# Kernel tuning notes

Hardware: AMD Instinct MI355X
Metric: run time of the kernel (lower is better)

## Reference

```python
import jax, jax.numpy as jnp
import numpy as np

# Architecture constants (from LocalGLMnet defaults)
LOOK_BACK, N_AGES, PAD = 10, 100, 2
KH, KW = 5, 5
H_OUT, W_OUT = LOOK_BACK + 2 * PAD - KH + 1, N_AGES + 2 * PAD - KW + 1  # 10, 100
ETA, ALPHA = 0.01, 0.0  # Ridge penalty
BATCH = 16384


def setup_inputs() -> dict:
    key = jax.random.key(0)
    k1, k2 = jax.random.split(key)
    x = jax.random.normal(k1, (BATCH, LOOK_BACK, N_AGES), dtype=jnp.float32)
    # unshared locally-connected weight (H_out, W_out, kH, kW); channels are 1 and squeezed
    weight = jax.random.normal(k2, (H_OUT, W_OUT, KH, KW), dtype=jnp.float32) * 0.01
    return {"x": x, "weight": weight}


def _locally_connected(x_pad, weight):
    # x_pad: (B, H_pad, W_pad); weight: (H_out, W_out, kH, kW)
    # out[b,i,j] = sum_{di,dj} x_pad[b,i+di,j+dj] * weight[i,j,di,dj]
    # Loop only over the fixed 5x5 kernel taps (25 fused shifted multiplies),
    # avoiding materialization of a (B, H_out, W_out, 25) patch tensor.
    out = jnp.zeros((x_pad.shape[0], H_OUT, W_OUT), dtype=x_pad.dtype)
    for di in range(KH):
        for dj in range(KW):
            out = out + x_pad[:, di:di + H_OUT, dj:dj + W_OUT] * weight[:, :, di, dj]
    return jax.nn.sigmoid(out)


def reference(x, weight):
    # x: (B, look_back, n_ages)
    x_pad = jnp.pad(x, ((0, 0), (PAD, PAD), (PAD, PAD)))
    interim = _locally_connected(x_pad, weight)        # (B, 10, 100) attention coeffs
    decoded = x * interim
    forecast = jnp.sum(decoded, axis=1, keepdims=True)  # (B, 1, 100)
    eps = 1e-6
    pen = ETA * ALPHA * jnp.sqrt(interim * interim + eps) \
        + ETA * (1.0 - ALPHA) * (interim * interim)
    penalty = jnp.sum(pen, axis=1, keepdims=True)       # (B, 1, 100)
    return jnp.concatenate([forecast, penalty], axis=1)  # (B, 2, 100)
```

## Files before the change

### kernel.cpp

```cpp
#include <hip/hip_runtime.h>


#define L2E 1.44269504088896340736f

__device__ __forceinline__ float fast_sigmoid(float s) {
    float e = __builtin_amdgcn_exp2f(s * (-L2E));
    return __builtin_amdgcn_rcpf(1.0f + e);
}

#define G_DECL(S) \
    float s##S##0=0.f,s##S##1=0.f,s##S##2=0.f,s##S##3=0.f,s##S##4=0.f, \
          s##S##5=0.f,s##S##6=0.f,s##S##7=0.f,s##S##8=0.f,s##S##9=0.f; \
    float f##S=0.f, p##S=0.f, cen1##S=0.f, cen2##S=0.f; \
    float xr##S##0, xr##S##1, xr##S##2, xr##S##3, xr##S##4;

#define G_LOADROW(S, R) { \
    const float* rp_ = x##S + (R) * 100; \
    xr##S##0 = v0 ? rp_[c0] : 0.f; \
    xr##S##1 = v1 ? rp_[c1] : 0.f; \
    xr##S##2 = rp_[c2]; \
    xr##S##3 = v3 ? rp_[c3] : 0.f; \
    xr##S##4 = v4 ? rp_[c4] : 0.f; }

#define G_LOADALL(R) G_LOADROW(A,R) G_LOADROW(B,R) G_LOADROW(C,R) G_LOADROW(D,R)

#define G_ACC_(S, I) \
    s##S##I = fmaf(xr##S##4, w4_, fmaf(xr##S##3, w3_, fmaf(xr##S##2, w2_, \
              fmaf(xr##S##1, w1_, fmaf(xr##S##0, w0_, s##S##I)))));
#define G_ACC(S, I) G_ACC_(S, I)

#define G_TAP(DI, I) { \
    const float* wp_ = wj + (I) * 1250 + (DI) * 5; \
    const float w0_=wp_[0], w1_=wp_[1], w2_=wp_[2], w3_=wp_[3], w4_=wp_[4]; \
    G_ACC(A, I) G_ACC(B, I) G_ACC(C, I) G_ACC(D, I) }

#define G_FIN1_(S, I, CEN) { \
    float itm_ = fast_sigmoid(s##S##I); \
    f##S = fmaf(CEN, itm_, f##S); \
    p##S = fmaf(0.01f * itm_, itm_, p##S); }
#define G_FIN1(S, I, CEN) G_FIN1_(S, I, CEN)

#define G_FINALL(I) G_FIN1(A,I,cen2A) G_FIN1(B,I,cen2B) G_FIN1(C,I,cen2C) G_FIN1(D,I,cen2D)

#define G_SHIFT(S) cen2##S = cen1##S; cen1##S = xr##S##2;
#define G_SHIFTALL() G_SHIFT(A) G_SHIFT(B) G_SHIFT(C) G_SHIFT(D)

__global__ __launch_bounds__(256)
void glm_fused(const float* __restrict__ x, const float* __restrict__ w,
               float* __restrict__ out) {
    __shared__ float wl[12500];

    const int tid = threadIdx.x;
    const int jh  = blockIdx.x & 1;
    const int blk = blockIdx.x >> 1;

    {
        const float2* __restrict__ src = (const float2*)w;
        float2* dst = (float2*)wl;
        for (int u = tid; u < 6250; u += 256) {
            int i  = u / 625;
            int r2 = u - i * 625;
            dst[i * 625 + r2] = src[i * 1250 + jh * 625 + r2];
        }
    }
    __syncthreads();

    const int tl = blk * 256 + tid;
    const int jl = tl % 50;
    const int bg = tl / 50;
    const int j  = jh * 50 + jl;

    const float* __restrict__ xA = x + bg * 4000;
    const float* __restrict__ xB = xA + 1000;
    const float* __restrict__ xC = xA + 2000;
    const float* __restrict__ xD = xA + 3000;
    const float* __restrict__ wj = wl + jl * 25;

    const bool v0 = (j >= 2), v1 = (j >= 1), v3 = (j <= 98), v4 = (j <= 97);
    const int c0 = v0 ? j - 2 : 0;
    const int c1 = v1 ? j - 1 : 0;
    const int c2 = j;
    const int c3 = v3 ? j + 1 : 0;
    const int c4 = v4 ? j + 2 : 0;

    G_DECL(A) G_DECL(B) G_DECL(C) G_DECL(D)

    G_LOADALL(0) G_TAP(0,2) G_TAP(1,1) G_TAP(2,0)                               G_SHIFTALL()
    G_LOADALL(1) G_TAP(0,3) G_TAP(1,2) G_TAP(2,1) G_TAP(3,0)                    G_SHIFTALL()
    G_LOADALL(2) G_TAP(0,4) G_TAP(1,3) G_TAP(2,2) G_TAP(3,1) G_TAP(4,0) G_FINALL(0) G_SHIFTALL()
    G_LOADALL(3) G_TAP(0,5) G_TAP(1,4) G_TAP(2,3) G_TAP(3,2) G_TAP(4,1) G_FINALL(1) G_SHIFTALL()
    G_LOADALL(4) G_TAP(0,6) G_TAP(1,5) G_TAP(2,4) G_TAP(3,3) G_TAP(4,2) G_FINALL(2) G_SHIFTALL()
    G_LOADALL(5) G_TAP(0,7) G_TAP(1,6) G_TAP(2,5) G_TAP(3,4) G_TAP(4,3) G_FINALL(3) G_SHIFTALL()
    G_LOADALL(6) G_TAP(0,8) G_TAP(1,7) G_TAP(2,6) G_TAP(3,5) G_TAP(4,4) G_FINALL(4) G_SHIFTALL()
    G_LOADALL(7) G_TAP(0,9) G_TAP(1,8) G_TAP(2,7) G_TAP(3,6) G_TAP(4,5) G_FINALL(5) G_SHIFTALL()
    G_LOADALL(8)            G_TAP(1,9) G_TAP(2,8) G_TAP(3,7) G_TAP(4,6) G_FINALL(6) G_SHIFTALL()
    G_LOADALL(9)                       G_TAP(2,9) G_TAP(3,8) G_TAP(4,7) G_FINALL(7) G_SHIFTALL()
    G_FIN1(A,8,cen2A) G_FIN1(B,8,cen2B) G_FIN1(C,8,cen2C) G_FIN1(D,8,cen2D)
    G_FIN1(A,9,cen1A) G_FIN1(B,9,cen1B) G_FIN1(C,9,cen1C) G_FIN1(D,9,cen1D)

    float* ob = out + bg * 800 + j;
    ob[0]   = fA;  ob[100] = pA;
    ob[200] = fB;  ob[300] = pB;
    ob[400] = fC;  ob[500] = pC;
    ob[600] = fD;  ob[700] = pD;
}

extern "C" void kernel_launch(void* const* d_in, const int* in_sizes, int n_in,
                              void* d_out, int out_size, void* d_ws, size_t ws_size,
                              hipStream_t stream) {
    const float* x = (const float*)d_in[0];
    const float* w = (const float*)d_in[1];
    float* out = (float*)d_out;
    dim3 grid(1600), block(256);
    hipLaunchKernelGGL(glm_fused, grid, block, 0, stream, x, w, out);
}
```

Measured before the change: 161.3 us.

## Split columns into quarters, fold edge masks into weights, double-buffer row loads

```diff
diff --git a/kernel.cpp b/kernel.cpp
--- a/kernel.cpp
+++ b/kernel.cpp
@@ -8,101 +8,101 @@
     return __builtin_amdgcn_rcpf(1.0f + e);
 }
 
-#define G_DECL(S) \
-    float s##S##0=0.f,s##S##1=0.f,s##S##2=0.f,s##S##3=0.f,s##S##4=0.f, \
-          s##S##5=0.f,s##S##6=0.f,s##S##7=0.f,s##S##8=0.f,s##S##9=0.f; \
-    float f##S=0.f, p##S=0.f, cen1##S=0.f, cen2##S=0.f; \
-    float xr##S##0, xr##S##1, xr##S##2, xr##S##3, xr##S##4;
+#define P_LOAD_(P, R) \
+    xA0##P = aA0[(R)*100]; xA1##P = aA1[(R)*100]; xA2##P = aA2[(R)*100]; \
+    xA3##P = aA3[(R)*100]; xA4##P = aA4[(R)*100]; \
+    xB0##P = aB0[(R)*100]; xB1##P = aB1[(R)*100]; xB2##P = aB2[(R)*100]; \
+    xB3##P = aB3[(R)*100]; xB4##P = aB4[(R)*100];
+#define P_LOAD(P, R) P_LOAD_(P, R)
 
-#define G_LOADROW(S, R) { \
-    const float* rp_ = x##S + (R) * 100; \
-    xr##S##0 = v0 ? rp_[c0] : 0.f; \
-    xr##S##1 = v1 ? rp_[c1] : 0.f; \
-    xr##S##2 = rp_[c2]; \
-    xr##S##3 = v3 ? rp_[c3] : 0.f; \
-    xr##S##4 = v4 ? rp_[c4] : 0.f; }
+#define G_TAP_(P, DI, I) { \
+    const float4 w4_ = W4p[(I)*125 + (DI)]; \
+    const float  we_ = W1p[(I)*125 + (DI)]; \
+    sA##I = fmaf(xA4##P, we_, fmaf(xA3##P, w4_.w, fmaf(xA2##P, w4_.z, \
+            fmaf(xA1##P, w4_.y, fmaf(xA0##P, w4_.x, sA##I))))); \
+    sB##I = fmaf(xB4##P, we_, fmaf(xB3##P, w4_.w, fmaf(xB2##P, w4_.z, \
+            fmaf(xB1##P, w4_.y, fmaf(xB0##P, w4_.x, sB##I))))); }
+#define G_TAP(P, DI, I) G_TAP_(P, DI, I)
 
-#define G_LOADALL(R) G_LOADROW(A,R) G_LOADROW(B,R) G_LOADROW(C,R) G_LOADROW(D,R)
+#define G_FIN_(I, CA, CB) { \
+    float tA_ = fast_sigmoid(sA##I); fA = fmaf(CA, tA_, fA); pA = fmaf(0.01f*tA_, tA_, pA); \
+    float tB_ = fast_sigmoid(sB##I); fB = fmaf(CB, tB_, fB); pB = fmaf(0.01f*tB_, tB_, pB); }
+#define G_FIN(I, CA, CB) G_FIN_(I, CA, CB)
 
-#define G_ACC_(S, I) \
-    s##S##I = fmaf(xr##S##4, w4_, fmaf(xr##S##3, w3_, fmaf(xr##S##2, w2_, \
-              fmaf(xr##S##1, w1_, fmaf(xr##S##0, w0_, s##S##I)))));
-#define G_ACC(S, I) G_ACC_(S, I)
-
-#define G_TAP(DI, I) { \
-    const float* wp_ = wj + (I) * 1250 + (DI) * 5; \
-    const float w0_=wp_[0], w1_=wp_[1], w2_=wp_[2], w3_=wp_[3], w4_=wp_[4]; \
-    G_ACC(A, I) G_ACC(B, I) G_ACC(C, I) G_ACC(D, I) }
-
-#define G_FIN1_(S, I, CEN) { \
-    float itm_ = fast_sigmoid(s##S##I); \
-    f##S = fmaf(CEN, itm_, f##S); \
-    p##S = fmaf(0.01f * itm_, itm_, p##S); }
-#define G_FIN1(S, I, CEN) G_FIN1_(S, I, CEN)
-
-#define G_FINALL(I) G_FIN1(A,I,cen2A) G_FIN1(B,I,cen2B) G_FIN1(C,I,cen2C) G_FIN1(D,I,cen2D)
-
-#define G_SHIFT(S) cen2##S = cen1##S; cen1##S = xr##S##2;
-#define G_SHIFTALL() G_SHIFT(A) G_SHIFT(B) G_SHIFT(C) G_SHIFT(D)
+#define G_SH_(P) cen2A = cen1A; cen1A = xA2##P; cen2B = cen1B; cen1B = xB2##P;
+#define G_SH(P) G_SH_(P)
 
 __global__ __launch_bounds__(256)
 void glm_fused(const float* __restrict__ x, const float* __restrict__ w,
                float* __restrict__ out) {
-    __shared__ float wl[12500];
+    __shared__ float4 W4s[1250];
+    __shared__ float  W1s[1250];
 
-    const int tid = threadIdx.x;
-    const int jh  = blockIdx.x & 1;
-    const int blk = blockIdx.x >> 1;
+    const int tid   = threadIdx.x;
+    const int q     = blockIdx.x & 3;
+    const int jbase = q * 25;
 
-    {
-        const float2* __restrict__ src = (const float2*)w;
-        float2* dst = (float2*)wl;
-        for (int u = tid; u < 6250; u += 256) {
-            int i  = u / 625;
-            int r2 = u - i * 625;
-            dst[i * 625 + r2] = src[i * 1250 + jh * 625 + r2];
-        }
+    for (int e = tid; e < 1250; e += 256) {
+        int i   = e / 125;
+        int r   = e - i * 125;
+        int jls = r / 5;
+        int di  = r - jls * 5;
+        int js  = jbase + jls;
+        const float* wp = w + i * 2500 + js * 25 + di * 5;
+        float w0 = (js >= 2) ? wp[0] : 0.f;
+        float w1 = (js >= 1) ? wp[1] : 0.f;
+        float w2 = wp[2];
+        float w3 = (js <= 98) ? wp[3] : 0.f;
+        float w4 = (js <= 97) ? wp[4] : 0.f;
+        W4s[e] = make_float4(w0, w1, w2, w3);
+        W1s[e] = w4;
     }
     __syncthreads();
 
-    const int tl = blk * 256 + tid;
-    const int jl = tl % 50;
-    const int bg = tl / 50;
-    const int j  = jh * 50 + jl;
+    const int t  = (blockIdx.x >> 2) * 256 + tid;
+    const int jl = t % 25;
+    const int bg = t / 25;
+    const int j  = jbase + jl;
 
-    const float* __restrict__ xA = x + bg * 4000;
-    const float* __restrict__ xB = xA + 1000;
-    const float* __restrict__ xC = xA + 2000;
-    const float* __restrict__ xD = xA + 3000;
-    const float* __restrict__ wj = wl + jl * 25;
+    const float4* W4p = W4s + jl * 5;
+    const float*  W1p = W1s + jl * 5;
 
-    const bool v0 = (j >= 2), v1 = (j >= 1), v3 = (j <= 98), v4 = (j <= 97);
-    const int c0 = v0 ? j - 2 : 0;
-    const int c1 = v1 ? j - 1 : 0;
+    const float* xA = x + bg * 2000;
+    const float* xB = xA + 1000;
+    const int c0 = (j >= 2) ? j - 2 : 0;
+    const int c1 = (j >= 1) ? j - 1 : 0;
     const int c2 = j;
-    const int c3 = v3 ? j + 1 : 0;
-    const int c4 = v4 ? j + 2 : 0;
+    const int c3 = (j <= 98) ? j + 1 : 99;
+    const int c4 = (j <= 97) ? j + 2 : 99;
+    const float* aA0 = xA + c0; const float* aA1 = xA + c1; const float* aA2 = xA + c2;
+    const float* aA3 = xA + c3; const float* aA4 = xA + c4;
+    const float* aB0 = xB + c0; const float* aB1 = xB + c1; const float* aB2 = xB + c2;
+    const float* aB3 = xB + c3; const float* aB4 = xB + c4;
 
-    G_DECL(A) G_DECL(B) G_DECL(C) G_DECL(D)
+    float sA0=0.f,sA1=0.f,sA2=0.f,sA3=0.f,sA4=0.f,sA5=0.f,sA6=0.f,sA7=0.f,sA8=0.f,sA9=0.f;
+    float sB0=0.f,sB1=0.f,sB2=0.f,sB3=0.f,sB4=0.f,sB5=0.f,sB6=0.f,sB7=0.f,sB8=0.f,sB9=0.f;
+    float fA=0.f,pA=0.f,fB=0.f,pB=0.f;
+    float cen1A=0.f,cen2A=0.f,cen1B=0.f,cen2B=0.f;
+    float xA0E,xA1E,xA2E,xA3E,xA4E,xB0E,xB1E,xB2E,xB3E,xB4E;
+    float xA0O,xA1O,xA2O,xA3O,xA4O,xB0O,xB1O,xB2O,xB3O,xB4O;
 
-    G_LOADALL(0) G_TAP(0,2) G_TAP(1,1) G_TAP(2,0)                               G_SHIFTALL()
-    G_LOADALL(1) G_TAP(0,3) G_TAP(1,2) G_TAP(2,1) G_TAP(3,0)                    G_SHIFTALL()
-    G_LOADALL(2) G_TAP(0,4) G_TAP(1,3) G_TAP(2,2) G_TAP(3,1) G_TAP(4,0) G_FINALL(0) G_SHIFTALL()
-    G_LOADALL(3) G_TAP(0,5) G_TAP(1,4) G_TAP(2,3) G_TAP(3,2) G_TAP(4,1) G_FINALL(1) G_SHIFTALL()
-    G_LOADALL(4) G_TAP(0,6) G_TAP(1,5) G_TAP(2,4) G_TAP(3,3) G_TAP(4,2) G_FINALL(2) G_SHIFTALL()
-    G_LOADALL(5) G_TAP(0,7) G_TAP(1,6) G_TAP(2,5) G_TAP(3,4) G_TAP(4,3) G_FINALL(3) G_SHIFTALL()
-    G_LOADALL(6) G_TAP(0,8) G_TAP(1,7) G_TAP(2,6) G_TAP(3,5) G_TAP(4,4) G_FINALL(4) G_SHIFTALL()
-    G_LOADALL(7) G_TAP(0,9) G_TAP(1,8) G_TAP(2,7) G_TAP(3,6) G_TAP(4,5) G_FINALL(5) G_SHIFTALL()
-    G_LOADALL(8)            G_TAP(1,9) G_TAP(2,8) G_TAP(3,7) G_TAP(4,6) G_FINALL(6) G_SHIFTALL()
-    G_LOADALL(9)                       G_TAP(2,9) G_TAP(3,8) G_TAP(4,7) G_FINALL(7) G_SHIFTALL()
-    G_FIN1(A,8,cen2A) G_FIN1(B,8,cen2B) G_FIN1(C,8,cen2C) G_FIN1(D,8,cen2D)
-    G_FIN1(A,9,cen1A) G_FIN1(B,9,cen1B) G_FIN1(C,9,cen1C) G_FIN1(D,9,cen1D)
+    P_LOAD(E,0)
+    P_LOAD(O,1) G_TAP(E,0,2) G_TAP(E,1,1) G_TAP(E,2,0)                                        G_SH(E)
+    P_LOAD(E,2) G_TAP(O,0,3) G_TAP(O,1,2) G_TAP(O,2,1) G_TAP(O,3,0)                           G_SH(O)
+    P_LOAD(O,3) G_TAP(E,0,4) G_TAP(E,1,3) G_TAP(E,2,2) G_TAP(E,3,1) G_TAP(E,4,0) G_FIN(0,cen2A,cen2B) G_SH(E)
+    P_LOAD(E,4) G_TAP(O,0,5) G_TAP(O,1,4) G_TAP(O,2,3) G_TAP(O,3,2) G_TAP(O,4,1) G_FIN(1,cen2A,cen2B) G_SH(O)
+    P_LOAD(O,5) G_TAP(E,0,6) G_TAP(E,1,5) G_TAP(E,2,4) G_TAP(E,3,3) G_TAP(E,4,2) G_FIN(2,cen2A,cen2B) G_SH(E)
+    P_LOAD(E,6) G_TAP(O,0,7) G_TAP(O,1,6) G_TAP(O,2,5) G_TAP(O,3,4) G_TAP(O,4,3) G_FIN(3,cen2A,cen2B) G_SH(O)
+    P_LOAD(O,7) G_TAP(E,0,8) G_TAP(E,1,7) G_TAP(E,2,6) G_TAP(E,3,5) G_TAP(E,4,4) G_FIN(4,cen2A,cen2B) G_SH(E)
+    P_LOAD(E,8) G_TAP(O,0,9) G_TAP(O,1,8) G_TAP(O,2,7) G_TAP(O,3,6) G_TAP(O,4,5) G_FIN(5,cen2A,cen2B) G_SH(O)
+    P_LOAD(O,9) G_TAP(E,1,9) G_TAP(E,2,8) G_TAP(E,3,7) G_TAP(E,4,6)              G_FIN(6,cen2A,cen2B) G_SH(E)
+                G_TAP(O,2,9) G_TAP(O,3,8) G_TAP(O,4,7)                           G_FIN(7,cen2A,cen2B) G_SH(O)
+    G_FIN(8, cen2A, cen2B)
+    G_FIN(9, cen1A, cen1B)
 
-    float* ob = out + bg * 800 + j;
+    float* ob = out + bg * 400 + j;
     ob[0]   = fA;  ob[100] = pA;
     ob[200] = fB;  ob[300] = pB;
-    ob[400] = fC;  ob[500] = pC;
-    ob[600] = fD;  ob[700] = pD;
 }
 
 extern "C" void kernel_launch(void* const* d_in, const int* in_sizes, int n_in,
@@ -111,6 +111,6 @@
     const float* x = (const float*)d_in[0];
     const float* w = (const float*)d_in[1];
     float* out = (float*)d_out;
-    dim3 grid(1600), block(256);
+    dim3 grid(3200), block(256);
     hipLaunchKernelGGL(glm_fused, grid, block, 0, stream, x, w, out);
 }
```

Result: faster. 132.3 us (-18.0%).

## Stage x tile in LDS and read weights as wave-uniform scalars

Applied to the files above, without the earlier changes.

```diff
diff --git a/kernel.cpp b/kernel.cpp
--- a/kernel.cpp
+++ b/kernel.cpp
@@ -8,101 +8,87 @@
     return __builtin_amdgcn_rcpf(1.0f + e);
 }
 
-#define G_DECL(S) \
-    float s##S##0=0.f,s##S##1=0.f,s##S##2=0.f,s##S##3=0.f,s##S##4=0.f, \
-          s##S##5=0.f,s##S##6=0.f,s##S##7=0.f,s##S##8=0.f,s##S##9=0.f; \
-    float f##S=0.f, p##S=0.f, cen1##S=0.f, cen2##S=0.f; \
-    float xr##S##0, xr##S##1, xr##S##2, xr##S##3, xr##S##4;
+#define XW_DECL \
+    float xw00,xw01,xw02,xw03,xw04, xw10,xw11,xw12,xw13,xw14, \
+          xw20,xw21,xw22,xw23,xw24, xw30,xw31,xw32,xw33,xw34, \
+          xw40,xw41,xw42,xw43,xw44;
 
-#define G_LOADROW(S, R) { \
-    const float* rp_ = x##S + (R) * 100; \
-    xr##S##0 = v0 ? rp_[c0] : 0.f; \
-    xr##S##1 = v1 ? rp_[c1] : 0.f; \
-    xr##S##2 = rp_[c2]; \
-    xr##S##3 = v3 ? rp_[c3] : 0.f; \
-    xr##S##4 = v4 ? rp_[c4] : 0.f; }
+#define XLOAD_(S, R) \
+    xw##S##0 = xr[(R)*780];       xw##S##1 = xr[(R)*780 + 65]; \
+    xw##S##2 = xr[(R)*780 + 130]; xw##S##3 = xr[(R)*780 + 195]; \
+    xw##S##4 = xr[(R)*780 + 260];
+#define XLOAD(S, R) XLOAD_(S, R)
 
-#define G_LOADALL(R) G_LOADROW(A,R) G_LOADROW(B,R) G_LOADROW(C,R) G_LOADROW(D,R)
+#define TAP_(I, DI, S) { \
+    const float* wp_ = wj + (I)*2500 + (DI)*5; \
+    acc = fmaf(xw##S##4, wp_[4], fmaf(xw##S##3, wp_[3], fmaf(xw##S##2, wp_[2], \
+          fmaf(xw##S##1, wp_[1], fmaf(xw##S##0, wp_[0], acc))))); }
+#define TAP(I, DI, S) TAP_(I, DI, S)
 
-#define G_ACC_(S, I) \
-    s##S##I = fmaf(xr##S##4, w4_, fmaf(xr##S##3, w3_, fmaf(xr##S##2, w2_, \
-              fmaf(xr##S##1, w1_, fmaf(xr##S##0, w0_, s##S##I)))));
-#define G_ACC(S, I) G_ACC_(S, I)
+#define FIN_(I, S) { \
+    float itm_ = fast_sigmoid(acc); acc = 0.f; \
+    fo = fmaf(xw##S##2, itm_, fo); pe = fmaf(itm_, itm_, pe); }
+#define FIN(I, S) FIN_(I, S)
 
-#define G_TAP(DI, I) { \
-    const float* wp_ = wj + (I) * 1250 + (DI) * 5; \
-    const float w0_=wp_[0], w1_=wp_[1], w2_=wp_[2], w3_=wp_[3], w4_=wp_[4]; \
-    G_ACC(A, I) G_ACC(B, I) G_ACC(C, I) G_ACC(D, I) }
-
-#define G_FIN1_(S, I, CEN) { \
-    float itm_ = fast_sigmoid(s##S##I); \
-    f##S = fmaf(CEN, itm_, f##S); \
-    p##S = fmaf(0.01f * itm_, itm_, p##S); }
-#define G_FIN1(S, I, CEN) G_FIN1_(S, I, CEN)
-
-#define G_FINALL(I) G_FIN1(A,I,cen2A) G_FIN1(B,I,cen2B) G_FIN1(C,I,cen2C) G_FIN1(D,I,cen2D)
-
-#define G_SHIFT(S) cen2##S = cen1##S; cen1##S = xr##S##2;
-#define G_SHIFTALL() G_SHIFT(A) G_SHIFT(B) G_SHIFT(C) G_SHIFT(D)
-
-__global__ __launch_bounds__(256)
+__global__ __launch_bounds__(256, 5)
 void glm_fused(const float* __restrict__ x, const float* __restrict__ w,
                float* __restrict__ out) {
-    __shared__ float wl[12500];
+    __shared__ float xs[7800];
 
     const int tid = threadIdx.x;
-    const int jh  = blockIdx.x & 1;
-    const int blk = blockIdx.x >> 1;
+    const int qj  = blockIdx.x % 25;
+    const int bt  = blockIdx.x / 25;
+    const int cb  = qj * 4 - 4;
+    const int bb  = bt * 64;
 
-    {
-        const float2* __restrict__ src = (const float2*)w;
-        float2* dst = (float2*)wl;
-        for (int u = tid; u < 6250; u += 256) {
-            int i  = u / 625;
-            int r2 = u - i * 625;
-            dst[i * 625 + r2] = src[i * 1250 + jh * 625 + r2];
+#pragma unroll
+    for (int k = 0; k < 8; ++k) {
+        int u = tid + (k << 8);
+        if (u < 1920) {
+            int b   = u / 30;
+            int rc  = u - b * 30;
+            int r   = rc / 3;
+            int c4  = rc - r * 3;
+            int col0 = cb + (c4 << 2);
+            bool ok  = (unsigned)col0 <= 96u;
+            int colc = ok ? col0 : 0;
+            const float4 v0 = *(const float4*)(x + (bb + b) * 1000 + r * 100 + colc);
+            float vx = ok ? v0.x : 0.f, vy = ok ? v0.y : 0.f;
+            float vz = ok ? v0.z : 0.f, vw = ok ? v0.w : 0.f;
+            int base = (r * 12 + (c4 << 2)) * 65 + b;
+            xs[base]       = vx;
+            xs[base + 65]  = vy;
+            xs[base + 130] = vz;
+            xs[base + 195] = vw;
         }
     }
     __syncthreads();
 
-    const int tl = blk * 256 + tid;
-    const int jl = tl % 50;
-    const int bg = tl / 50;
-    const int j  = jh * 50 + jl;
+    const int lane = tid & 63;
+    const int wid  = tid >> 6;
+    const int j = __builtin_amdgcn_readfirstlane(qj * 4 + wid);
+    const float* __restrict__ wj = w + j * 25;
+    const float* __restrict__ xr = xs + (wid + 2) * 65 + lane;
 
-    const float* __restrict__ xA = x + bg * 4000;
-    const float* __restrict__ xB = xA + 1000;
-    const float* __restrict__ xC = xA + 2000;
-    const float* __restrict__ xD = xA + 3000;
-    const float* __restrict__ wj = wl + jl * 25;
+    XW_DECL
+    float acc = 0.f, fo = 0.f, pe = 0.f;
 
-    const bool v0 = (j >= 2), v1 = (j >= 1), v3 = (j <= 98), v4 = (j <= 97);
-    const int c0 = v0 ? j - 2 : 0;
-    const int c1 = v1 ? j - 1 : 0;
-    const int c2 = j;
-    const int c3 = v3 ? j + 1 : 0;
-    const int c4 = v4 ? j + 2 : 0;
+    XLOAD(0, 0) XLOAD(1, 1) XLOAD(2, 2)
 
-    G_DECL(A) G_DECL(B) G_DECL(C) G_DECL(D)
+     XLOAD(3, 3) TAP(0,2,0) TAP(0,3,1) TAP(0,4,2)                       FIN(0, 0)
+     XLOAD(4, 4) TAP(1,1,0) TAP(1,2,1) TAP(1,3,2) TAP(1,4,3)            FIN(1, 1)
+     TAP(2,0,0) XLOAD(0, 5) TAP(2,1,1) TAP(2,2,2) TAP(2,3,3) TAP(2,4,4) FIN(2, 2)
+     TAP(3,0,1) XLOAD(1, 6) TAP(3,1,2) TAP(3,2,3) TAP(3,3,4) TAP(3,4,0) FIN(3, 3)
+     TAP(4,0,2) XLOAD(2, 7) TAP(4,1,3) TAP(4,2,4) TAP(4,3,0) TAP(4,4,1) FIN(4, 4)
+     TAP(5,0,3) XLOAD(3, 8) TAP(5,1,4) TAP(5,2,0) TAP(5,3,1) TAP(5,4,2) FIN(5, 0)
+     TAP(6,0,4) XLOAD(4, 9) TAP(6,1,0) TAP(6,2,1) TAP(6,3,2) TAP(6,4,3) FIN(6, 1)
+     TAP(7,0,0) TAP(7,1,1) TAP(7,2,2) TAP(7,3,3) TAP(7,4,4)             FIN(7, 2)
+     TAP(8,0,1) TAP(8,1,2) TAP(8,2,3) TAP(8,3,4)                        FIN(8, 3)
+     TAP(9,0,2) TAP(9,1,3) TAP(9,2,4)                                   FIN(9, 4)
 
-    G_LOADALL(0) G_TAP(0,2) G_TAP(1,1) G_TAP(2,0)                               G_SHIFTALL()
-    G_LOADALL(1) G_TAP(0,3) G_TAP(1,2) G_TAP(2,1) G_TAP(3,0)                    G_SHIFTALL()
-    G_LOADALL(2) G_TAP(0,4) G_TAP(1,3) G_TAP(2,2) G_TAP(3,1) G_TAP(4,0) G_FINALL(0) G_SHIFTALL()
-    G_LOADALL(3) G_TAP(0,5) G_TAP(1,4) G_TAP(2,3) G_TAP(3,2) G_TAP(4,1) G_FINALL(1) G_SHIFTALL()
-    G_LOADALL(4) G_TAP(0,6) G_TAP(1,5) G_TAP(2,4) G_TAP(3,3) G_TAP(4,2) G_FINALL(2) G_SHIFTALL()
-    G_LOADALL(5) G_TAP(0,7) G_TAP(1,6) G_TAP(2,5) G_TAP(3,4) G_TAP(4,3) G_FINALL(3) G_SHIFTALL()
-    G_LOADALL(6) G_TAP(0,8) G_TAP(1,7) G_TAP(2,6) G_TAP(3,5) G_TAP(4,4) G_FINALL(4) G_SHIFTALL()
-    G_LOADALL(7) G_TAP(0,9) G_TAP(1,8) G_TAP(2,7) G_TAP(3,6) G_TAP(4,5) G_FINALL(5) G_SHIFTALL()
-    G_LOADALL(8)            G_TAP(1,9) G_TAP(2,8) G_TAP(3,7) G_TAP(4,6) G_FINALL(6) G_SHIFTALL()
-    G_LOADALL(9)                       G_TAP(2,9) G_TAP(3,8) G_TAP(4,7) G_FINALL(7) G_SHIFTALL()
-    G_FIN1(A,8,cen2A) G_FIN1(B,8,cen2B) G_FIN1(C,8,cen2C) G_FIN1(D,8,cen2D)
-    G_FIN1(A,9,cen1A) G_FIN1(B,9,cen1B) G_FIN1(C,9,cen1C) G_FIN1(D,9,cen1D)
-
-    float* ob = out + bg * 800 + j;
-    ob[0]   = fA;  ob[100] = pA;
-    ob[200] = fB;  ob[300] = pB;
-    ob[400] = fC;  ob[500] = pC;
-    ob[600] = fD;  ob[700] = pD;
+    float* ob = out + (bb + lane) * 200 + j;
+    ob[0]   = fo;
+    ob[100] = 0.01f * pe;
 }
 
 extern "C" void kernel_launch(void* const* d_in, const int* in_sizes, int n_in,
@@ -111,6 +97,6 @@
     const float* x = (const float*)d_in[0];
     const float* w = (const float*)d_in[1];
     float* out = (float*)d_out;
-    dim3 grid(1600), block(256);
+    dim3 grid(6400), block(256);
     hipLaunchKernelGGL(glm_fused, grid, block, 0, stream, x, w, out);
 }
```

Result: slower. 169.0 us (+4.8%).
